# Kernel optimization log

Measured on AMD Instinct MI355X. Metric: run time of the kernel, lower is better.

## Reference

```python
import jax, jax.numpy as jnp
import numpy as np

EPS = 1e-05
MARGIN = 0.0


def setup_inputs() -> dict:
    key = jax.random.key(0)
    k1, k2 = jax.random.split(key)
    embeddings = jax.random.normal(k1, (512, 512), dtype=jnp.float32)
    labels = jax.random.randint(k2, (512,), 0, 32, dtype=jnp.int64)
    return {"embeddings": embeddings, "labels": labels}


def _pairwise_distance(e, squared=False):
    # e: [B, D] -> [B, B] euclidean distances
    dot = jnp.matmul(e, e.T)
    sq = jnp.diag(dot)
    d = sq[:, None] - 2.0 * dot + sq[None, :]
    d = jnp.maximum(d, 0.0)
    if not squared:
        zmask = (d == 0.0).astype(d.dtype)
        d = d + zmask * EPS
        d = jnp.sqrt(d) + EPS
        d = d * (1.0 - zmask)
    return d


def _triplet_mask(labels):
    B = labels.shape[0]
    not_eq = ~jnp.eye(B, dtype=bool)
    # distinct indices i != j, i != k, j != k  -> [B, B, B]
    distinct = not_eq[:, :, None] & not_eq[:, None, :] & not_eq[None, :, :]
    lab_eq = labels[None, :] == labels[:, None]  # symmetric [B, B]
    valid = lab_eq[:, :, None] & (~lab_eq[:, None, :])  # label[i]==label[j], label[i]!=label[k]
    return (distinct & valid).astype(jnp.float32)


def reference(embeddings, labels):
    d = _pairwise_distance(embeddings, squared=False)  # [B, B]
    # triplet_loss[a, p, n] = d[a, p] - d[a, n] + margin
    tl = d[:, :, None] - d[:, None, :] + MARGIN
    mask = _triplet_mask(labels)
    tl = jnp.maximum(mask * tl, 0.0)
    num_positive = jnp.sum((tl > 1e-05).astype(jnp.float32))
    num_valid = jnp.sum(mask)
    fraction_positive = num_positive / (num_valid + 1e-05)
    loss = jnp.sum(tl) / (num_positive + 1e-05)
    return (loss, fraction_positive)
```

## Files before the change

kernel.cpp:

```cpp
#include <hip/hip_runtime.h>

#define BSZ  512
#define EPSF 1e-5f
#define KT   64
#define NS   8
#define TT   64
#define LSTR 76

#define WS_PARTIAL 8
#define WS_P       2048

__device__ __forceinline__ float dist_xform(float v) {
    v = fmaxf(v, 0.0f);
    float z = (v == 0.0f) ? 1.0f : 0.0f;
    v = sqrtf(v + z * EPSF) + EPSF;
    return v * (1.0f - z);
}

__global__ __launch_bounds__(256) void dsq_kernel(const float* __restrict__ E,
                                                  float* __restrict__ ws) {
    __shared__ __align__(16) float As[TT][LSTR];
    __shared__ __align__(16) float Bs[TT][LSTR];
    const int tid = threadIdx.x;
    const int bj = blockIdx.x * TT;
    const int bi = blockIdx.y * TT;
    const int k0 = blockIdx.z * KT;

    {
        const int r0 = tid >> 4;
        const int kc = (tid & 15) * 4;
#pragma unroll
        for (int p = 0; p < 4; ++p) {
            const int row = p * 16 + r0;
            float4 va = *(const float4*)(E + (size_t)(bi + row) * BSZ + k0 + kc);
            float4 vb = *(const float4*)(E + (size_t)(bj + row) * BSZ + k0 + kc);
            *(float4*)&As[row][kc] = va;
            *(float4*)&Bs[row][kc] = vb;
        }
    }
    __syncthreads();

    const int tx = tid & 15;
    const int ty = tid >> 4;
    float acc[4][4];
#pragma unroll
    for (int r = 0; r < 4; ++r)
#pragma unroll
        for (int c = 0; c < 4; ++c) acc[r][c] = 0.0f;

#pragma unroll 4
    for (int k4 = 0; k4 < KT / 4; ++k4) {
        float4 Af[4], Bf[4];
#pragma unroll
        for (int r = 0; r < 4; ++r) Af[r] = *(const float4*)&As[ty * 4 + r][k4 * 4];
#pragma unroll
        for (int c = 0; c < 4; ++c) Bf[c] = *(const float4*)&Bs[tx * 4 + c][k4 * 4];
#pragma unroll
        for (int r = 0; r < 4; ++r)
#pragma unroll
            for (int c = 0; c < 4; ++c) {
                float d;
                d = Af[r].x - Bf[c].x; acc[r][c] = fmaf(d, d, acc[r][c]);
                d = Af[r].y - Bf[c].y; acc[r][c] = fmaf(d, d, acc[r][c]);
                d = Af[r].z - Bf[c].z; acc[r][c] = fmaf(d, d, acc[r][c]);
                d = Af[r].w - Bf[c].w; acc[r][c] = fmaf(d, d, acc[r][c]);
            }
    }

    float* Pp = ws + WS_P + (size_t)blockIdx.z * BSZ * BSZ;
#pragma unroll
    for (int r = 0; r < 4; ++r) {
        float4 v = {acc[r][0], acc[r][1], acc[r][2], acc[r][3]};
        *(float4*)(Pp + (size_t)(bi + ty * 4 + r) * BSZ + bj + tx * 4) = v;
    }
}

__global__ __launch_bounds__(256) void triplet_kernel(const int* __restrict__ labels,
                                                      const float* __restrict__ ws,
                                                      float* __restrict__ partial) {
    const int a = blockIdx.x;
    const int tid = threadIdx.x;
    __shared__ float drow[BSZ];
    __shared__ int   lab[BSZ];
    __shared__ int   poslist[BSZ];
    __shared__ int   npos_s;
    __shared__ float wsum[4];
    __shared__ int   wcnt[4];

    if (tid == 0) npos_s = 0;
    for (int t = tid; t < BSZ; t += 256) lab[t] = labels[t];

    const float* P = ws + WS_P;
    {
        float2 s2 = {0.f, 0.f};
#pragma unroll
        for (int s = 0; s < NS; ++s) {
            float2 v = *(const float2*)(P + ((size_t)s * BSZ + a) * BSZ + tid * 2);
            s2.x += v.x; s2.y += v.y;
        }
        drow[tid * 2 + 0] = dist_xform(s2.x);
        drow[tid * 2 + 1] = dist_xform(s2.y);
    }
    __syncthreads();

    const int la = lab[a];
    for (int t = tid; t < BSZ; t += 256) {
        if (lab[t] == la && t != a) {
            int idx = atomicAdd(&npos_s, 1);
            poslist[idx] = t;
        }
    }
    __syncthreads();

    const int npos = npos_s;
    const int nneg = BSZ - 1 - npos;
    float sum = 0.0f;
    int   cnt = 0;
    const int total = npos * BSZ;
    for (int idx = tid; idx < total; idx += 256) {
        const int p = poslist[idx >> 9];
        const int n = idx & (BSZ - 1);
        if (lab[n] != la) {
            const float v = drow[p] - drow[n];
            if (v > 0.0f)  sum += v;
            if (v > 1e-5f) cnt++;
        }
    }
#pragma unroll
    for (int off = 32; off > 0; off >>= 1) {
        sum += __shfl_down(sum, off);
        cnt += __shfl_down(cnt, off);
    }
    const int wave = tid >> 6, lane = tid & 63;
    if (lane == 0) { wsum[wave] = sum; wcnt[wave] = cnt; }
    __syncthreads();
    if (tid == 0) {
        partial[a]           = wsum[0] + wsum[1] + wsum[2] + wsum[3];
        partial[BSZ + a]     = (float)(wcnt[0] + wcnt[1] + wcnt[2] + wcnt[3]);
        partial[2*BSZ + a]   = (float)npos * (float)nneg;
    }
}

__global__ __launch_bounds__(256) void final_kernel(const float* __restrict__ partial,
                                                    float* __restrict__ out) {
    const int tid = threadIdx.x;
    float s = partial[tid]         + partial[tid + 256];
    float c = partial[BSZ + tid]   + partial[BSZ + tid + 256];
    float v = partial[2*BSZ + tid] + partial[2*BSZ + tid + 256];
#pragma unroll
    for (int off = 32; off > 0; off >>= 1) {
        s += __shfl_down(s, off);
        c += __shfl_down(c, off);
        v += __shfl_down(v, off);
    }
    __shared__ float ws_[4], wc[4], wv[4];
    const int wave = tid >> 6, lane = tid & 63;
    if (lane == 0) { ws_[wave] = s; wc[wave] = c; wv[wave] = v; }
    __syncthreads();
    if (tid == 0) {
        float S = ws_[0] + ws_[1] + ws_[2] + ws_[3];
        float C = wc[0] + wc[1] + wc[2] + wc[3];
        float V = wv[0] + wv[1] + wv[2] + wv[3];
        out[0] = S / (C + 1e-5f);
        out[1] = C / (V + 1e-5f);
    }
}

extern "C" void kernel_launch(void* const* d_in, const int* in_sizes, int n_in,
                              void* d_out, int out_size, void* d_ws, size_t ws_size,
                              hipStream_t stream) {
    const float* E      = (const float*)d_in[0];
    const int*   labels = (const int*)d_in[1];
    float* out = (float*)d_out;
    float* ws  = (float*)d_ws;
    float* partial = ws + WS_PARTIAL;

    dsq_kernel<<<dim3(8, 8, NS), 256, 0, stream>>>(E, ws);
    triplet_kernel<<<BSZ, 256, 0, stream>>>(labels, ws, partial);
    final_kernel<<<1, 256, 0, stream>>>(partial, out);
}
```

Before: 80.19 us.

## Fuse final reduction into triplet kernel and split distance K dimension finer

Drops the separate final reduction launch: each triplet block publishes its partials and bumps a global counter, and the last block to finish does the grand reduction. The counter is reset inside the first distance block. The distance kernel also halves its K tile and doubles the number of K splits, giving 1024 blocks instead of 512, at the cost of writing and re-reading twice as many partial distance matrices in the triplet kernel.

```diff
diff --git a/kernel.cpp b/kernel.cpp
--- a/kernel.cpp
+++ b/kernel.cpp
@@ -2,10 +2,10 @@
 
 #define BSZ  512
 #define EPSF 1e-5f
-#define KT   64
-#define NS   8
+#define KT   32
+#define NS   16
 #define TT   64
-#define LSTR 76
+#define LSTR 36
 
 #define WS_PARTIAL 8
 #define WS_P       2048
@@ -19,6 +19,9 @@
 
 __global__ __launch_bounds__(256) void dsq_kernel(const float* __restrict__ E,
                                                   float* __restrict__ ws) {
+    if (blockIdx.x == 0 && blockIdx.y == 0 && blockIdx.z == 0 && threadIdx.x == 0)
+        ((int*)ws)[0] = 0;
+
     __shared__ __align__(16) float As[TT][LSTR];
     __shared__ __align__(16) float Bs[TT][LSTR];
     const int tid = threadIdx.x;
@@ -27,11 +30,11 @@
     const int k0 = blockIdx.z * KT;
 
     {
-        const int r0 = tid >> 4;
-        const int kc = (tid & 15) * 4;
+        const int g  = tid >> 3;
+        const int kc = (tid & 7) * 4;
 #pragma unroll
-        for (int p = 0; p < 4; ++p) {
-            const int row = p * 16 + r0;
+        for (int p = 0; p < 2; ++p) {
+            const int row = p * 32 + g;
             float4 va = *(const float4*)(E + (size_t)(bi + row) * BSZ + k0 + kc);
             float4 vb = *(const float4*)(E + (size_t)(bj + row) * BSZ + k0 + kc);
             *(float4*)&As[row][kc] = va;
@@ -48,7 +51,7 @@
 #pragma unroll
         for (int c = 0; c < 4; ++c) acc[r][c] = 0.0f;
 
-#pragma unroll 4
+#pragma unroll
     for (int k4 = 0; k4 < KT / 4; ++k4) {
         float4 Af[4], Bf[4];
 #pragma unroll
@@ -76,8 +79,8 @@
 }
 
 __global__ __launch_bounds__(256) void triplet_kernel(const int* __restrict__ labels,
-                                                      const float* __restrict__ ws,
-                                                      float* __restrict__ partial) {
+                                                      float* __restrict__ ws,
+                                                      float* __restrict__ out) {
     const int a = blockIdx.x;
     const int tid = threadIdx.x;
     __shared__ float drow[BSZ];
@@ -86,6 +89,8 @@
     __shared__ int   npos_s;
     __shared__ float wsum[4];
     __shared__ int   wcnt[4];
+    __shared__ float wcf[4], wvf[4];
+    __shared__ int   is_last;
 
     if (tid == 0) npos_s = 0;
     for (int t = tid; t < BSZ; t += 256) lab[t] = labels[t];
@@ -134,35 +139,38 @@
     const int wave = tid >> 6, lane = tid & 63;
     if (lane == 0) { wsum[wave] = sum; wcnt[wave] = cnt; }
     __syncthreads();
+
+    float* partial = ws + WS_PARTIAL;
     if (tid == 0) {
         partial[a]           = wsum[0] + wsum[1] + wsum[2] + wsum[3];
         partial[BSZ + a]     = (float)(wcnt[0] + wcnt[1] + wcnt[2] + wcnt[3]);
         partial[2*BSZ + a]   = (float)npos * (float)nneg;
+        __threadfence();
+        unsigned old = atomicAdd((unsigned*)ws, 1u);
+        is_last = (old == BSZ - 1) ? 1 : 0;
     }
-}
+    __syncthreads();
 
-__global__ __launch_bounds__(256) void final_kernel(const float* __restrict__ partial,
-                                                    float* __restrict__ out) {
-    const int tid = threadIdx.x;
-    float s = partial[tid]         + partial[tid + 256];
-    float c = partial[BSZ + tid]   + partial[BSZ + tid + 256];
-    float v = partial[2*BSZ + tid] + partial[2*BSZ + tid + 256];
+    if (is_last) {
+        __threadfence();
+        float s = partial[tid]         + partial[tid + 256];
+        float c = partial[BSZ + tid]   + partial[BSZ + tid + 256];
+        float v = partial[2*BSZ + tid] + partial[2*BSZ + tid + 256];
 #pragma unroll
-    for (int off = 32; off > 0; off >>= 1) {
-        s += __shfl_down(s, off);
-        c += __shfl_down(c, off);
-        v += __shfl_down(v, off);
-    }
-    __shared__ float ws_[4], wc[4], wv[4];
-    const int wave = tid >> 6, lane = tid & 63;
-    if (lane == 0) { ws_[wave] = s; wc[wave] = c; wv[wave] = v; }
-    __syncthreads();
-    if (tid == 0) {
-        float S = ws_[0] + ws_[1] + ws_[2] + ws_[3];
-        float C = wc[0] + wc[1] + wc[2] + wc[3];
-        float V = wv[0] + wv[1] + wv[2] + wv[3];
-        out[0] = S / (C + 1e-5f);
-        out[1] = C / (V + 1e-5f);
+        for (int off = 32; off > 0; off >>= 1) {
+            s += __shfl_down(s, off);
+            c += __shfl_down(c, off);
+            v += __shfl_down(v, off);
+        }
+        if (lane == 0) { wsum[wave] = s; wcf[wave] = c; wvf[wave] = v; }
+        __syncthreads();
+        if (tid == 0) {
+            float S = wsum[0] + wsum[1] + wsum[2] + wsum[3];
+            float C = wcf[0] + wcf[1] + wcf[2] + wcf[3];
+            float V = wvf[0] + wvf[1] + wvf[2] + wvf[3];
+            out[0] = S / (C + 1e-5f);
+            out[1] = C / (V + 1e-5f);
+        }
     }
 }
 
@@ -173,9 +181,7 @@
     const int*   labels = (const int*)d_in[1];
     float* out = (float*)d_out;
     float* ws  = (float*)d_ws;
-    float* partial = ws + WS_PARTIAL;
 
     dsq_kernel<<<dim3(8, 8, NS), 256, 0, stream>>>(E, ws);
-    triplet_kernel<<<BSZ, 256, 0, stream>>>(labels, ws, partial);
-    final_kernel<<<1, 256, 0, stream>>>(partial, out);
+    triplet_kernel<<<BSZ, 256, 0, stream>>>(labels, ws, out);
 }
```

New measurement: 94.10 us. 17.3% more time.
